# Optimization experiments

Measured on AMD Instinct MI355X. Metric: run time of the kernel, lower is better.

## Reference

```python
import jax, jax.numpy as jnp
import numpy as np

B, S, DIM, H = 8, 1024, 1024, 16
HID = 512  # FeedForward default hidden_dim=512 (module passes only dim)
DH = DIM // H
EPS = 1e-5


def setup_inputs() -> dict:
    key = jax.random.key(0)
    ks = jax.random.split(key, 12)
    s = 1.0 / np.sqrt(DIM)
    return {
        "x": jax.random.normal(ks[0], (B, S, DIM), dtype=jnp.float32),
        "Wq": jax.random.normal(ks[1], (DIM, DIM), dtype=jnp.float32) * s,
        "Wk": jax.random.normal(ks[2], (DIM, DIM), dtype=jnp.float32) * s,
        "Wv": jax.random.normal(ks[3], (DIM, DIM), dtype=jnp.float32) * s,
        "Wo": jax.random.normal(ks[4], (DIM, DIM), dtype=jnp.float32) * s,
        "ln1_g": jnp.ones((DIM,), jnp.float32),
        "ln1_b": jnp.zeros((DIM,), jnp.float32),
        "W1": jax.random.normal(ks[5], (DIM, HID), dtype=jnp.float32) * s,
        "b1": jnp.zeros((HID,), jnp.float32),
        "W2": jax.random.normal(ks[6], (HID, DIM), dtype=jnp.float32) * (1.0 / np.sqrt(HID)),
        "b2": jnp.zeros((DIM,), jnp.float32),
        "ln2_g": jnp.ones((DIM,), jnp.float32),
        "ln2_b": jnp.zeros((DIM,), jnp.float32),
    }


def _layer_norm(x, g, b):
    mu = jnp.mean(x, axis=-1, keepdims=True)
    var = jnp.mean(jnp.square(x - mu), axis=-1, keepdims=True)
    return (x - mu) * jax.lax.rsqrt(var + EPS) * g + b


def reference(x, Wq, Wk, Wv, Wo, ln1_g, ln1_b, W1, b1, W2, b2, ln2_g, ln2_b):
    # Multi-head self-attention (dropout = identity at eval)
    def heads(t):  # [B,S,DIM] -> [B,H,S,DH]
        return t.reshape(B, S, H, DH).transpose(0, 2, 1, 3)

    q = heads(x @ Wq)
    k = heads(x @ Wk)
    v = heads(x @ Wv)
    scores = jnp.einsum("bhqd,bhkd->bhqk", q, k) / jnp.sqrt(jnp.float32(DH))
    attn = jax.nn.softmax(scores, axis=-1)
    ctx = jnp.einsum("bhqk,bhkd->bhqd", attn, v)
    ctx = ctx.transpose(0, 2, 1, 3).reshape(B, S, DIM)
    mha = ctx @ Wo

    h = _layer_norm(mha + x, ln1_g, ln1_b)
    ff = jax.nn.relu(h @ W1 + b1) @ W2 + b2
    out = _layer_norm(ff + h, ln2_g, ln2_b)
    return out
```

## Files before the change

kernel.cpp:

```cpp
#include <hip/hip_runtime.h>
#include <cstdint>
#include <cstddef>

#define DEV __device__ __forceinline__

typedef __bf16 bf16x8 __attribute__((ext_vector_type(8)));
typedef __bf16 bf16x4 __attribute__((ext_vector_type(4)));
typedef short  short4v __attribute__((ext_vector_type(4)));
typedef float  f32x4  __attribute__((ext_vector_type(4)));

static constexpr int Bb  = 8;
static constexpr int S   = 1024;
static constexpr int DIM = 1024;
static constexpr int H   = 16;
static constexpr int DH  = 64;
static constexpr int HID = 512;
static constexpr int M   = Bb * S;

DEV uint16_t f2bf(float f) {
  union { float f; uint32_t u; } v; v.f = f;
  uint32_t r = v.u + 0x7fffu + ((v.u >> 16) & 1u);
  return (uint16_t)(r >> 16);
}
DEV float bf2f(uint32_t u) {
  union { uint32_t u; float f; } v; v.u = u << 16;
  return v.f;
}

DEV void gl_lds16(const uint16_t* g, uint16_t* lds) {
  __builtin_amdgcn_global_load_lds(
      (const __attribute__((address_space(1))) void*)g,
      (__attribute__((address_space(3))) void*)lds, 16, 0, 0);
}

DEV bf16x8 ld8(const uint16_t* p) { return *reinterpret_cast<const bf16x8*>(p); }

#if __has_builtin(__builtin_amdgcn_mfma_f32_16x16x16bf16_1k)
DEV f32x4 mfma16(bf16x4 a, bf16x4 b, f32x4 c) {
  return __builtin_amdgcn_mfma_f32_16x16x16bf16_1k(
      __builtin_bit_cast(short4v, a), __builtin_bit_cast(short4v, b), c, 0, 0, 0);
}
#else
DEV f32x4 mfma16(bf16x4 a, bf16x4 b, f32x4 c) {
  asm volatile("v_mfma_f32_16x16x16_bf16 %0, %1, %2, %0" : "+v"(c) : "v"(a), "v"(b));
  return c;
}
#endif

DEV int swz(int row, int col) {
  return row * 64 + (((col >> 3) ^ (row & 7)) << 3) + (col & 7);
}

__global__ __launch_bounds__(256) void cvt_f32_bf16(const float* __restrict__ in,
                                                    uint16_t* __restrict__ out, int n) {
  int i = (blockIdx.x * 256 + threadIdx.x) * 8;
  if (i >= n) return;
  const float4* p = reinterpret_cast<const float4*>(in + i);
  float4 a = p[0], b = p[1];
  uint16_t o[8] = {f2bf(a.x), f2bf(a.y), f2bf(a.z), f2bf(a.w),
                   f2bf(b.x), f2bf(b.y), f2bf(b.z), f2bf(b.w)};
  uint4 pk;
  pk.x = (uint32_t)o[0] | ((uint32_t)o[1] << 16);
  pk.y = (uint32_t)o[2] | ((uint32_t)o[3] << 16);
  pk.z = (uint32_t)o[4] | ((uint32_t)o[5] << 16);
  pk.w = (uint32_t)o[6] | ((uint32_t)o[7] << 16);
  *reinterpret_cast<uint4*>(out + i) = pk;
}

__global__ __launch_bounds__(256) void transpose_cvt(const float* __restrict__ in,
                                                     uint16_t* __restrict__ out,
                                                     int R, int C) {
  __shared__ float tile[32][33];
  int c0 = blockIdx.x * 32, r0 = blockIdx.y * 32;
  int tx = threadIdx.x, ty = threadIdx.y;
  #pragma unroll
  for (int i = 0; i < 4; i++)
    tile[ty + i * 8][tx] = in[(size_t)(r0 + ty + i * 8) * C + c0 + tx];
  __syncthreads();
  #pragma unroll
  for (int i = 0; i < 4; i++)
    out[(size_t)(c0 + ty + i * 8) * R + r0 + tx] = f2bf(tile[tx][ty + i * 8]);
}

__global__ __launch_bounds__(256) void vtrans(const uint16_t* __restrict__ qkv,
                                              uint16_t* __restrict__ vt) {
  int bh = blockIdx.x;
  int s0 = blockIdx.y * 64;
  int b = bh >> 4, h = bh & 15;
  int tid = threadIdx.x;
  __shared__ uint16_t t[64][65];
  #pragma unroll
  for (int j = 0; j < 16; j++) {
    int lin = j * 256 + tid;
    int sl = lin >> 6, d = lin & 63;
    t[d][sl] = qkv[(size_t)(b * S + s0 + sl) * 3072 + 2048 + h * 64 + d];
  }
  __syncthreads();
  #pragma unroll
  for (int j = 0; j < 16; j++) {
    int lin = j * 256 + tid;
    int dl = lin >> 6, sl = lin & 63;
    vt[((size_t)bh * 64 + dl) * S + s0 + sl] = t[dl][sl];
  }
}

template <int BIAS, int RELU, int OUT_BF16>
__global__ __launch_bounds__(256) void gemm_bt(const uint16_t* __restrict__ A,
                                               const uint16_t* __restrict__ Bt,
                                               const float* __restrict__ bias,
                                               void* __restrict__ Cout,
                                               int Mm, int N, int K) {
  __shared__ __align__(16) uint16_t As[128 * 32];
  __shared__ __align__(16) uint16_t Bs[128 * 32];
  const int tid = threadIdx.x;
  const int w = tid >> 6, l = tid & 63;
  int nwg = gridDim.x * gridDim.y;
  int lin = blockIdx.y * gridDim.x + blockIdx.x;
  if (!(nwg & 7)) lin = (lin & 7) * (nwg >> 3) + (lin >> 3);
  const int bx = lin % gridDim.x, by = lin / gridDim.x;
  const int m0 = by * 128, n0 = bx * 128;
  const int wr = (w >> 1) * 64, wc = (w & 1) * 64;
  const int wbase = w * 64;
  f32x4 acc[4][4] = {};
  const uint16_t* Ag = A + (size_t)m0 * K;
  const uint16_t* Bg = Bt + (size_t)n0 * K;

  for (int k0 = 0; k0 < K; k0 += 32) {
    __syncthreads();
    #pragma unroll
    for (int n = 0; n < 2; n++) {
      int lin2 = n * 256 + tid;
      int row = lin2 >> 2, col = (lin2 & 3) * 8;
      gl_lds16(Ag + (size_t)row * K + k0 + col, &As[(size_t)(n * 256 + wbase) * 8]);
      gl_lds16(Bg + (size_t)row * K + k0 + col, &Bs[(size_t)(n * 256 + wbase) * 8]);
    }
    __syncthreads();
    bf16x8 af[4], bfr[4];
    #pragma unroll
    for (int i = 0; i < 4; i++) {
      af[i]  = ld8(&As[(wr + i * 16 + (l & 15)) * 32 + (l >> 4) * 8]);
      bfr[i] = ld8(&Bs[(wc + i * 16 + (l & 15)) * 32 + (l >> 4) * 8]);
    }
    #pragma unroll
    for (int i = 0; i < 4; i++)
      #pragma unroll
      for (int j = 0; j < 4; j++)
        acc[i][j] = __builtin_amdgcn_mfma_f32_16x16x32_bf16(af[i], bfr[j], acc[i][j], 0, 0, 0);
  }

  const int r0 = m0 + wr + (l >> 4) * 4;
  const int c0 = n0 + wc + (l & 15);
  #pragma unroll
  for (int j = 0; j < 4; j++) {
    int col = c0 + j * 16;
    float bv = BIAS ? bias[col] : 0.0f;
    #pragma unroll
    for (int i = 0; i < 4; i++) {
      #pragma unroll
      for (int r = 0; r < 4; r++) {
        float v = acc[i][j][r] + bv;
        if (RELU) v = fmaxf(v, 0.0f);
        int row = r0 + i * 16 + r;
        if (OUT_BF16)
          ((uint16_t*)Cout)[(size_t)row * N + col] = f2bf(v);
        else
          ((float*)Cout)[(size_t)row * N + col] = v;
      }
    }
  }
}

__global__ __launch_bounds__(512, 2) void gemm256(const uint16_t* __restrict__ A,
                                                  const uint16_t* __restrict__ Bt,
                                                  uint16_t* __restrict__ Cout,
                                                  int N, int K) {
  __shared__ __align__(16) uint16_t As[2][256 * 64];
  __shared__ __align__(16) uint16_t Bs[2][256 * 64];
  const int tid = threadIdx.x;
  const int w = tid >> 6, l = tid & 63;
  const int hi = l >> 4, c = l & 15;
  int nwg = gridDim.x * gridDim.y;
  int lin = blockIdx.y * gridDim.x + blockIdx.x;
  if (!(nwg & 7)) lin = (lin & 7) * (nwg >> 3) + (lin >> 3);
  const int bx = lin % gridDim.x, by = lin / gridDim.x;
  const int m0 = by * 256, n0 = bx * 256;
  const int wr = w >> 2, wc = w & 3;
  const uint16_t* Ag = A + (size_t)m0 * K;
  const uint16_t* Bg = Bt + (size_t)n0 * K;
  f32x4 acc[8][4] = {};

  const int srow = tid >> 3, sch = tid & 7;
  auto stage = [&](int k0, int buf) {
    #pragma unroll
    for (int i = 0; i < 4; i++) {
      int row = i * 64 + srow;
      int scol = (sch ^ (row & 7)) * 8;
      gl_lds16(Ag + (size_t)row * K + k0 + scol, &As[buf][(i * 512 + w * 64) * 8]);
    }
    #pragma unroll
    for (int i = 0; i < 4; i++) {
      int row = i * 64 + srow;
      int scol = (sch ^ (row & 7)) * 8;
      gl_lds16(Bg + (size_t)row * K + k0 + scol, &Bs[buf][(i * 512 + w * 64) * 8]);
    }
  };

  stage(0, 0);
  stage(64, 1);
  asm volatile("s_waitcnt vmcnt(8)" ::: "memory");
  __builtin_amdgcn_s_barrier();

  const int NTK = K >> 6;
  for (int t = 0; t < NTK; t++) {
    const int cur = t & 1;
    const uint16_t* Ab = As[cur];
    const uint16_t* Bb = Bs[cur];
    bf16x8 bfr[4][2];
    #pragma unroll
    for (int ni = 0; ni < 4; ni++)
      #pragma unroll
      for (int kk = 0; kk < 2; kk++)
        bfr[ni][kk] = ld8(&Bb[swz(wc * 64 + ni * 16 + c, kk * 32 + hi * 8)]);
    #pragma unroll
    for (int mi = 0; mi < 8; mi++) {
      bf16x8 a0 = ld8(&Ab[swz(wr * 128 + mi * 16 + c, hi * 8)]);
      bf16x8 a1 = ld8(&Ab[swz(wr * 128 + mi * 16 + c, 32 + hi * 8)]);
      #pragma unroll
      for (int ni = 0; ni < 4; ni++) {
        acc[mi][ni] = __builtin_amdgcn_mfma_f32_16x16x32_bf16(a0, bfr[ni][0], acc[mi][ni], 0, 0, 0);
        acc[mi][ni] = __builtin_amdgcn_mfma_f32_16x16x32_bf16(a1, bfr[ni][1], acc[mi][ni], 0, 0, 0);
      }
    }
    if (t == NTK - 1) break;
    asm volatile("s_waitcnt lgkmcnt(0)" ::: "memory");
    __builtin_amdgcn_s_barrier();
    if (t + 2 < NTK) {
      stage((t + 2) << 6, cur);
      asm volatile("s_waitcnt vmcnt(8)" ::: "memory");
    } else {
      asm volatile("s_waitcnt vmcnt(0)" ::: "memory");
    }
    __builtin_amdgcn_s_barrier();
  }

  const int r0 = m0 + wr * 128 + hi * 4;
  const int c0 = n0 + wc * 64 + c;
  #pragma unroll
  for (int mi = 0; mi < 8; mi++)
    #pragma unroll
    for (int ni = 0; ni < 4; ni++)
      #pragma unroll
      for (int r = 0; r < 4; r++)
        Cout[(size_t)(r0 + mi * 16 + r) * N + c0 + ni * 16] = f2bf(acc[mi][ni][r]);
}

__global__ __launch_bounds__(256, 4) void attn5(const uint16_t* __restrict__ qkv,
                                                const uint16_t* __restrict__ vt,
                                                uint16_t* __restrict__ ctx) {
  int blk = blockIdx.x;
  int xcd = blk & 7, idx = blk >> 3;
  int qt = idx & 7;
  int bh = xcd + 8 * (idx >> 3);
  int h = bh & 15, b = bh >> 4;
  int q0 = qt * 128;
  int tid = threadIdx.x;
  int w = tid >> 6, l = tid & 63;
  int hi = l >> 4, c = l & 15;

  __shared__ __align__(16) uint16_t Klds[2][64 * 64];
  __shared__ __align__(16) uint16_t Vlds[2][64 * 64];

  const uint16_t* qbase = qkv + (size_t)(b * S + q0 + w * 32) * 3072 + h * 64;
  bf16x8 aq[2][2];
  #pragma unroll
  for (int qg = 0; qg < 2; qg++)
    #pragma unroll
    for (int dk = 0; dk < 2; dk++)
      aq[qg][dk] = ld8(qbase + (size_t)(qg * 16 + c) * 3072 + dk * 32 + hi * 8);

  f32x4 acc[2][4] = {};
  float psum[2] = {};

  const uint16_t* kgbase = qkv + (size_t)(b * S) * 3072 + 1024 + h * 64;
  const uint16_t* vgbase = vt + (size_t)(b * 16 + h) * 64 * S;

  int srow = tid >> 3, sch = tid & 7;
  uint4 kreg[2], vreg[2];

  auto load_tiles = [&](int kt) {
    #pragma unroll
    for (int i = 0; i < 2; i++) {
      int row = srow + i * 32;
      kreg[i] = *(const uint4*)(kgbase + (size_t)(kt + row) * 3072 + sch * 8);
      vreg[i] = *(const uint4*)(vgbase + (size_t)row * S + kt + sch * 8);
    }
  };
  auto store_tiles = [&](int buf) {
    #pragma unroll
    for (int i = 0; i < 2; i++) {
      int row = srow + i * 32;
      *(uint4*)&Klds[buf][swz(row, sch * 8)] = kreg[i];
      *(uint4*)&Vlds[buf][swz(row, sch * 8)] = vreg[i];
    }
  };

  load_tiles(0);
  store_tiles(0);
  __syncthreads();

  constexpr float C2 = 0.125f * 1.44269504f;
  constexpr int NT = S / 64;
  for (int t = 0; t < NT; t++) {
    int cur = t & 1;
    if (t + 1 < NT) load_tiles((t + 1) * 64);

    #pragma unroll
    for (int kb = 0; kb < 4; kb++) {
      bf16x8 kf0 = ld8(&Klds[cur][swz(kb * 16 + c, hi * 8)]);
      bf16x8 kf1 = ld8(&Klds[cur][swz(kb * 16 + c, 32 + hi * 8)]);
      bf16x4 pb[2];
      #pragma unroll
      for (int qg = 0; qg < 2; qg++) {
        f32x4 z = {0.f, 0.f, 0.f, 0.f};
        z = __builtin_amdgcn_mfma_f32_16x16x32_bf16(kf0, aq[qg][0], z, 0, 0, 0);
        z = __builtin_amdgcn_mfma_f32_16x16x32_bf16(kf1, aq[qg][1], z, 0, 0, 0);
        #pragma unroll
        for (int r = 0; r < 4; r++) {
          float p = exp2f(z[r] * C2);
          psum[qg] += p;
          pb[qg][r] = (__bf16)p;
        }
      }
      #pragma unroll
      for (int db = 0; db < 4; db++) {
        bf16x4 va = *(const bf16x4*)&Vlds[cur][swz(db * 16 + c, kb * 16 + hi * 4)];
        acc[0][db] = mfma16(va, pb[0], acc[0][db]);
        acc[1][db] = mfma16(va, pb[1], acc[1][db]);
      }
    }

    if (t + 1 < NT) store_tiles(cur ^ 1);
    __syncthreads();
  }

  #pragma unroll
  for (int qg = 0; qg < 2; qg++) {
    psum[qg] += __shfl_xor(psum[qg], 16);
    psum[qg] += __shfl_xor(psum[qg], 32);
  }

  uint16_t* Bw = &Vlds[w >> 1][(w & 1) * 2048];
  #pragma unroll
  for (int qg = 0; qg < 2; qg++) {
    float inv = 1.0f / psum[qg];
    int q = qg * 16 + c;
    #pragma unroll
    for (int db = 0; db < 4; db++) {
      uint2 pk;
      pk.x = (uint32_t)f2bf(acc[qg][db][0] * inv) |
             ((uint32_t)f2bf(acc[qg][db][1] * inv) << 16);
      pk.y = (uint32_t)f2bf(acc[qg][db][2] * inv) |
             ((uint32_t)f2bf(acc[qg][db][3] * inv) << 16);
      int chunk4 = (db * 4 + hi) ^ (q & 15);
      *(uint2*)&Bw[q * 64 + chunk4 * 4] = pk;
    }
  }
  int rrow = l >> 3, rch = l & 7;
  size_t gq0 = (size_t)(b * S + q0 + w * 32);
  #pragma unroll
  for (int it = 0; it < 4; it++) {
    int row = it * 8 + rrow;
    int k0 = (2 * rch) ^ (row & 15);
    int base = (k0 & ~1) * 4;
    uint4 v = *(const uint4*)&Bw[row * 64 + base];
    if (row & 1) { uint32_t t0 = v.x, t1 = v.y; v.x = v.z; v.y = v.w; v.z = t0; v.w = t1; }
    *(uint4*)&ctx[(gq0 + row) * DIM + h * 64 + rch * 8] = v;
  }
}

__global__ __launch_bounds__(256) void ln1_b(const uint16_t* __restrict__ a16,
                                             const float* __restrict__ xres,
                                             const float* __restrict__ g,
                                             const float* __restrict__ beta,
                                             uint16_t* __restrict__ h16) {
  int row = blockIdx.x;
  int t = threadIdx.x;
  int w = t >> 6, l = t & 63;
  uint2 av = reinterpret_cast<const uint2*>(a16 + (size_t)row * DIM)[t];
  float4 xv = reinterpret_cast<const float4*>(xres + (size_t)row * DIM)[t];
  float v0 = bf2f(av.x & 0xffff) + xv.x;
  float v1 = bf2f(av.x >> 16)    + xv.y;
  float v2 = bf2f(av.y & 0xffff) + xv.z;
  float v3 = bf2f(av.y >> 16)    + xv.w;
  float s = v0 + v1 + v2 + v3;
  float sq = v0 * v0 + v1 * v1 + v2 * v2 + v3 * v3;
  #pragma unroll
  for (int off = 32; off >= 1; off >>= 1) {
    s += __shfl_xor(s, off);
    sq += __shfl_xor(sq, off);
  }
  __shared__ float ws[4], wq[4];
  if (l == 0) { ws[w] = s; wq[w] = sq; }
  __syncthreads();
  s = ws[0] + ws[1] + ws[2] + ws[3];
  sq = wq[0] + wq[1] + wq[2] + wq[3];
  float mu = s * (1.0f / DIM);
  float var = sq * (1.0f / DIM) - mu * mu;
  float rstd = rsqrtf(var + 1e-5f);
  const float4 gv = reinterpret_cast<const float4*>(g)[t];
  const float4 btv = reinterpret_cast<const float4*>(beta)[t];
  float o0 = (v0 - mu) * rstd * gv.x + btv.x;
  float o1 = (v1 - mu) * rstd * gv.y + btv.y;
  float o2 = (v2 - mu) * rstd * gv.z + btv.z;
  float o3 = (v3 - mu) * rstd * gv.w + btv.w;
  uint2 pk;
  pk.x = (uint32_t)f2bf(o0) | ((uint32_t)f2bf(o1) << 16);
  pk.y = (uint32_t)f2bf(o2) | ((uint32_t)f2bf(o3) << 16);
  reinterpret_cast<uint2*>(h16 + (size_t)row * DIM)[t] = pk;
}

__global__ __launch_bounds__(256) void ln2_b(const float* __restrict__ ff,
                                             const uint16_t* __restrict__ h16,
                                             const float* __restrict__ g,
                                             const float* __restrict__ beta,
                                             float* __restrict__ out_f) {
  int row = blockIdx.x;
  int t = threadIdx.x;
  int w = t >> 6, l = t & 63;
  float4 av = reinterpret_cast<const float4*>(ff + (size_t)row * DIM)[t];
  uint2 hv = reinterpret_cast<const uint2*>(h16 + (size_t)row * DIM)[t];
  float v0 = av.x + bf2f(hv.x & 0xffff);
  float v1 = av.y + bf2f(hv.x >> 16);
  float v2 = av.z + bf2f(hv.y & 0xffff);
  float v3 = av.w + bf2f(hv.y >> 16);
  float s = v0 + v1 + v2 + v3;
  float sq = v0 * v0 + v1 * v1 + v2 * v2 + v3 * v3;
  #pragma unroll
  for (int off = 32; off >= 1; off >>= 1) {
    s += __shfl_xor(s, off);
    sq += __shfl_xor(sq, off);
  }
  __shared__ float ws[4], wq[4];
  if (l == 0) { ws[w] = s; wq[w] = sq; }
  __syncthreads();
  s = ws[0] + ws[1] + ws[2] + ws[3];
  sq = wq[0] + wq[1] + wq[2] + wq[3];
  float mu = s * (1.0f / DIM);
  float var = sq * (1.0f / DIM) - mu * mu;
  float rstd = rsqrtf(var + 1e-5f);
  const float4 gv = reinterpret_cast<const float4*>(g)[t];
  const float4 btv = reinterpret_cast<const float4*>(beta)[t];
  float4 o;
  o.x = (v0 - mu) * rstd * gv.x + btv.x;
  o.y = (v1 - mu) * rstd * gv.y + btv.y;
  o.z = (v2 - mu) * rstd * gv.z + btv.z;
  o.w = (v3 - mu) * rstd * gv.w + btv.w;
  reinterpret_cast<float4*>(out_f + (size_t)row * DIM)[t] = o;
}

extern "C" void kernel_launch(void* const* d_in, const int* in_sizes, int n_in,
                              void* d_out, int out_size, void* d_ws, size_t ws_size,
                              hipStream_t stream) {
  const float* x    = (const float*)d_in[0];
  const float* Wq   = (const float*)d_in[1];
  const float* Wk   = (const float*)d_in[2];
  const float* Wv   = (const float*)d_in[3];
  const float* Wo   = (const float*)d_in[4];
  const float* ln1g = (const float*)d_in[5];
  const float* ln1b = (const float*)d_in[6];
  const float* W1   = (const float*)d_in[7];
  const float* b1   = (const float*)d_in[8];
  const float* W2   = (const float*)d_in[9];
  const float* b2   = (const float*)d_in[10];
  const float* ln2g = (const float*)d_in[11];
  const float* ln2b = (const float*)d_in[12];
  float* out = (float*)d_out;

  char* ws = (char*)d_ws;
  uint16_t* wqkv_t = (uint16_t*)(ws + 0);
  uint16_t* wo_t   = (uint16_t*)(ws + 6291456);
  uint16_t* w1_t   = (uint16_t*)(ws + 8388608);
  uint16_t* w2_t   = (uint16_t*)(ws + 9437184);
  uint16_t* x16    = (uint16_t*)(ws + 10485760);
  uint16_t* ctx16  = x16;
  uint16_t* qkv16  = (uint16_t*)(ws + 27262976);
  uint16_t* mha16  = (uint16_t*)(ws + 27262976);
  float*    ff2    = (float*)(ws + 27262976);
  uint16_t* h16    = (uint16_t*)(ws + 60817408);
  uint16_t* vt16   = (uint16_t*)(ws + 77594624);
  uint16_t* mid16  = vt16;

  cvt_f32_bf16<<<4096, 256, 0, stream>>>(x, x16, M * DIM);
  dim3 tb(32, 8);
  transpose_cvt<<<dim3(32, 32), tb, 0, stream>>>(Wq, wqkv_t,                 DIM, DIM);
  transpose_cvt<<<dim3(32, 32), tb, 0, stream>>>(Wk, wqkv_t + 1024 * 1024,   DIM, DIM);
  transpose_cvt<<<dim3(32, 32), tb, 0, stream>>>(Wv, wqkv_t + 2048 * 1024,   DIM, DIM);
  transpose_cvt<<<dim3(32, 32), tb, 0, stream>>>(Wo, wo_t,                   DIM, DIM);
  transpose_cvt<<<dim3(16, 32), tb, 0, stream>>>(W1, w1_t, DIM, HID);
  transpose_cvt<<<dim3(32, 16), tb, 0, stream>>>(W2, w2_t, HID, DIM);
  gemm256<<<dim3(12, 32), 512, 0, stream>>>(x16, wqkv_t, qkv16, 3072, DIM);
  vtrans<<<dim3(128, 16), 256, 0, stream>>>(qkv16, vt16);
  attn5<<<1024, 256, 0, stream>>>(qkv16, vt16, ctx16);
  gemm_bt<0, 0, 1><<<dim3(8, 64), 256, 0, stream>>>(ctx16, wo_t, nullptr, mha16, M, DIM, DIM);
  ln1_b<<<M, 256, 0, stream>>>(mha16, x, ln1g, ln1b, h16);
  gemm_bt<1, 1, 1><<<dim3(4, 64), 256, 0, stream>>>(h16, w1_t, b1, mid16, M, HID, DIM);
  gemm_bt<1, 0, 0><<<dim3(8, 64), 256, 0, stream>>>(mid16, w2_t, b2, ff2, M, DIM, HID);
  ln2_b<<<M, 256, 0, stream>>>(ff2, h16, ln2g, ln2b, out);
}
```

Baseline: 275.4 us.

## Stage attention K/V tiles via direct global-to-LDS loads with deeper prefetch

The attention kernel now copies K and V tiles straight from global memory into LDS through a gl_lds16 helper, skipping the register round trip, and prefetches two tiles ahead with explicit vmcnt waits and barriers. It also interleaves the two QK MFMA chains, raises wave priority around the MFMA blocks, and bumps launch bounds to 5 blocks per CU. The goal is to hide global load latency and free registers for higher occupancy. The hand-written waitcnt and barrier sequence must stay correct, and the swizzle now depends on the load layout matching the swz() read pattern.

```diff
diff --git a/kernel.cpp b/kernel.cpp
--- a/kernel.cpp
+++ b/kernel.cpp
@@ -254,7 +254,7 @@
         Cout[(size_t)(r0 + mi * 16 + r) * N + c0 + ni * 16] = f2bf(acc[mi][ni][r]);
 }
 
-__global__ __launch_bounds__(256, 4) void attn5(const uint16_t* __restrict__ qkv,
+__global__ __launch_bounds__(256, 5) void attn6(const uint16_t* __restrict__ qkv,
                                                 const uint16_t* __restrict__ vt,
                                                 uint16_t* __restrict__ ctx) {
   int blk = blockIdx.x;
@@ -284,63 +284,71 @@
   const uint16_t* kgbase = qkv + (size_t)(b * S) * 3072 + 1024 + h * 64;
   const uint16_t* vgbase = vt + (size_t)(b * 16 + h) * 64 * S;
 
-  int srow = tid >> 3, sch = tid & 7;
-  uint4 kreg[2], vreg[2];
-
-  auto load_tiles = [&](int kt) {
+  const int lr = l >> 3, lc = l & 7;
+  const int scol = (lc ^ lr) * 8;
+  auto stage = [&](int kt, int buf) {
     #pragma unroll
     for (int i = 0; i < 2; i++) {
-      int row = srow + i * 32;
-      kreg[i] = *(const uint4*)(kgbase + (size_t)(kt + row) * 3072 + sch * 8);
-      vreg[i] = *(const uint4*)(vgbase + (size_t)row * S + kt + sch * 8);
+      int slab = w * 2 + i;
+      gl_lds16(kgbase + (size_t)(kt + slab * 8 + lr) * 3072 + scol,
+               &Klds[buf][slab * 512]);
+      gl_lds16(vgbase + (size_t)(slab * 8 + lr) * S + kt + scol,
+               &Vlds[buf][slab * 512]);
     }
   };
-  auto store_tiles = [&](int buf) {
-    #pragma unroll
-    for (int i = 0; i < 2; i++) {
-      int row = srow + i * 32;
-      *(uint4*)&Klds[buf][swz(row, sch * 8)] = kreg[i];
-      *(uint4*)&Vlds[buf][swz(row, sch * 8)] = vreg[i];
-    }
-  };
-
-  load_tiles(0);
-  store_tiles(0);
-  __syncthreads();
+
+  stage(0, 0);
+  stage(64, 1);
+  asm volatile("s_waitcnt vmcnt(4)" ::: "memory");
+  __builtin_amdgcn_s_barrier();
 
   constexpr float C2 = 0.125f * 1.44269504f;
   constexpr int NT = S / 64;
   for (int t = 0; t < NT; t++) {
     int cur = t & 1;
-    if (t + 1 < NT) load_tiles((t + 1) * 64);
-
+    const uint16_t* Kc = Klds[cur];
+    const uint16_t* Vc = Vlds[cur];
     #pragma unroll
     for (int kb = 0; kb < 4; kb++) {
-      bf16x8 kf0 = ld8(&Klds[cur][swz(kb * 16 + c, hi * 8)]);
-      bf16x8 kf1 = ld8(&Klds[cur][swz(kb * 16 + c, 32 + hi * 8)]);
+      bf16x8 kf0 = ld8(&Kc[swz(kb * 16 + c, hi * 8)]);
+      bf16x8 kf1 = ld8(&Kc[swz(kb * 16 + c, 32 + hi * 8)]);
       bf16x4 pb[2];
-      #pragma unroll
-      for (int qg = 0; qg < 2; qg++) {
-        f32x4 z = {0.f, 0.f, 0.f, 0.f};
-        z = __builtin_amdgcn_mfma_f32_16x16x32_bf16(kf0, aq[qg][0], z, 0, 0, 0);
-        z = __builtin_amdgcn_mfma_f32_16x16x32_bf16(kf1, aq[qg][1], z, 0, 0, 0);
-        #pragma unroll
-        for (int r = 0; r < 4; r++) {
-          float p = exp2f(z[r] * C2);
-          psum[qg] += p;
-          pb[qg][r] = (__bf16)p;
-        }
+      __builtin_amdgcn_s_setprio(1);
+      f32x4 z0 = {0.f, 0.f, 0.f, 0.f}, z1 = {0.f, 0.f, 0.f, 0.f};
+      z0 = __builtin_amdgcn_mfma_f32_16x16x32_bf16(kf0, aq[0][0], z0, 0, 0, 0);
+      z0 = __builtin_amdgcn_mfma_f32_16x16x32_bf16(kf1, aq[0][1], z0, 0, 0, 0);
+      z1 = __builtin_amdgcn_mfma_f32_16x16x32_bf16(kf0, aq[1][0], z1, 0, 0, 0);
+      z1 = __builtin_amdgcn_mfma_f32_16x16x32_bf16(kf1, aq[1][1], z1, 0, 0, 0);
+      __builtin_amdgcn_s_setprio(0);
+      #pragma unroll
+      for (int r = 0; r < 4; r++) {
+        float p0 = exp2f(z0[r] * C2);
+        float p1 = exp2f(z1[r] * C2);
+        psum[0] += p0;
+        psum[1] += p1;
+        pb[0][r] = (__bf16)p0;
+        pb[1][r] = (__bf16)p1;
       }
+      __builtin_amdgcn_s_setprio(1);
       #pragma unroll
       for (int db = 0; db < 4; db++) {
-        bf16x4 va = *(const bf16x4*)&Vlds[cur][swz(db * 16 + c, kb * 16 + hi * 4)];
+        bf16x4 va = *(const bf16x4*)&Vc[swz(db * 16 + c, kb * 16 + hi * 4)];
         acc[0][db] = mfma16(va, pb[0], acc[0][db]);
         acc[1][db] = mfma16(va, pb[1], acc[1][db]);
       }
-    }
-
-    if (t + 1 < NT) store_tiles(cur ^ 1);
-    __syncthreads();
+      __builtin_amdgcn_s_setprio(0);
+    }
+
+    if (t == NT - 1) break;
+    asm volatile("s_waitcnt lgkmcnt(0)" ::: "memory");
+    __builtin_amdgcn_s_barrier();
+    if (t + 2 < NT) {
+      stage((t + 2) * 64, cur);
+      asm volatile("s_waitcnt vmcnt(4)" ::: "memory");
+    } else {
+      asm volatile("s_waitcnt vmcnt(0)" ::: "memory");
+    }
+    __builtin_amdgcn_s_barrier();
   }
 
   #pragma unroll
@@ -348,6 +356,8 @@
     psum[qg] += __shfl_xor(psum[qg], 16);
     psum[qg] += __shfl_xor(psum[qg], 32);
   }
+
+  __syncthreads();
 
   uint16_t* Bw = &Vlds[w >> 1][(w & 1) * 2048];
   #pragma unroll
@@ -500,7 +510,7 @@
   transpose_cvt<<<dim3(32, 16), tb, 0, stream>>>(W2, w2_t, HID, DIM);
   gemm256<<<dim3(12, 32), 512, 0, stream>>>(x16, wqkv_t, qkv16, 3072, DIM);
   vtrans<<<dim3(128, 16), 256, 0, stream>>>(qkv16, vt16);
-  attn5<<<1024, 256, 0, stream>>>(qkv16, vt16, ctx16);
+  attn6<<<1024, 256, 0, stream>>>(qkv16, vt16, ctx16);
   gemm_bt<0, 0, 1><<<dim3(8, 64), 256, 0, stream>>>(ctx16, wo_t, nullptr, mha16, M, DIM, DIM);
   ln1_b<<<M, 256, 0, stream>>>(mha16, x, ln1g, ln1b, h16);
   gemm_bt<1, 1, 1><<<dim3(4, 64), 256, 0, stream>>>(h16, w1_t, b1, mid16, M, HID, DIM);
```

Measured after the change: 286.9 us. +4.2%, slower.

## Halve attention query tile per block and store FFN output in bf16

Applied to the files above, without the earlier changes.

The attention kernel now gives each wave 16 queries instead of 32, so a block covers 64 queries and the launch grows to 2048 blocks, with occupancy raised to 5 blocks per CU. This cuts register pressure and adds parallelism, but every block reloads the full K/V stream, so K/V traffic doubles. Separately, the second FFN GEMM now writes bf16 instead of fp32 and the final layernorm reads bf16, halving that intermediate's memory traffic at some precision cost.

```diff
diff --git a/kernel.cpp b/kernel.cpp
--- a/kernel.cpp
+++ b/kernel.cpp
@@ -254,15 +254,15 @@
         Cout[(size_t)(r0 + mi * 16 + r) * N + c0 + ni * 16] = f2bf(acc[mi][ni][r]);
 }
 
-__global__ __launch_bounds__(256, 4) void attn5(const uint16_t* __restrict__ qkv,
+__global__ __launch_bounds__(256, 5) void attn7(const uint16_t* __restrict__ qkv,
                                                 const uint16_t* __restrict__ vt,
                                                 uint16_t* __restrict__ ctx) {
   int blk = blockIdx.x;
   int xcd = blk & 7, idx = blk >> 3;
-  int qt = idx & 7;
-  int bh = xcd + 8 * (idx >> 3);
+  int qt = idx & 15;
+  int bh = xcd + 8 * (idx >> 4);
   int h = bh & 15, b = bh >> 4;
-  int q0 = qt * 128;
+  int q0 = qt * 64;
   int tid = threadIdx.x;
   int w = tid >> 6, l = tid & 63;
   int hi = l >> 4, c = l & 15;
@@ -270,16 +270,14 @@
   __shared__ __align__(16) uint16_t Klds[2][64 * 64];
   __shared__ __align__(16) uint16_t Vlds[2][64 * 64];
 
-  const uint16_t* qbase = qkv + (size_t)(b * S + q0 + w * 32) * 3072 + h * 64;
-  bf16x8 aq[2][2];
-  #pragma unroll
-  for (int qg = 0; qg < 2; qg++)
-    #pragma unroll
-    for (int dk = 0; dk < 2; dk++)
-      aq[qg][dk] = ld8(qbase + (size_t)(qg * 16 + c) * 3072 + dk * 32 + hi * 8);
-
-  f32x4 acc[2][4] = {};
-  float psum[2] = {};
+  const uint16_t* qbase = qkv + (size_t)(b * S + q0 + w * 16) * 3072 + h * 64;
+  bf16x8 aq[2];
+  #pragma unroll
+  for (int dk = 0; dk < 2; dk++)
+    aq[dk] = ld8(qbase + (size_t)c * 3072 + dk * 32 + hi * 8);
+
+  f32x4 acc[4] = {};
+  float psum = 0.0f;
 
   const uint16_t* kgbase = qkv + (size_t)(b * S) * 3072 + 1024 + h * 64;
   const uint16_t* vgbase = vt + (size_t)(b * 16 + h) * 64 * S;
@@ -313,29 +311,27 @@
   for (int t = 0; t < NT; t++) {
     int cur = t & 1;
     if (t + 1 < NT) load_tiles((t + 1) * 64);
+    const uint16_t* Kc = Klds[cur];
+    const uint16_t* Vc = Vlds[cur];
 
     #pragma unroll
     for (int kb = 0; kb < 4; kb++) {
-      bf16x8 kf0 = ld8(&Klds[cur][swz(kb * 16 + c, hi * 8)]);
-      bf16x8 kf1 = ld8(&Klds[cur][swz(kb * 16 + c, 32 + hi * 8)]);
-      bf16x4 pb[2];
-      #pragma unroll
-      for (int qg = 0; qg < 2; qg++) {
-        f32x4 z = {0.f, 0.f, 0.f, 0.f};
-        z = __builtin_amdgcn_mfma_f32_16x16x32_bf16(kf0, aq[qg][0], z, 0, 0, 0);
-        z = __builtin_amdgcn_mfma_f32_16x16x32_bf16(kf1, aq[qg][1], z, 0, 0, 0);
-        #pragma unroll
-        for (int r = 0; r < 4; r++) {
-          float p = exp2f(z[r] * C2);
-          psum[qg] += p;
-          pb[qg][r] = (__bf16)p;
-        }
+      bf16x8 kf0 = ld8(&Kc[swz(kb * 16 + c, hi * 8)]);
+      bf16x8 kf1 = ld8(&Kc[swz(kb * 16 + c, 32 + hi * 8)]);
+      f32x4 z = {0.f, 0.f, 0.f, 0.f};
+      z = __builtin_amdgcn_mfma_f32_16x16x32_bf16(kf0, aq[0], z, 0, 0, 0);
+      z = __builtin_amdgcn_mfma_f32_16x16x32_bf16(kf1, aq[1], z, 0, 0, 0);
+      bf16x4 pb;
+      #pragma unroll
+      for (int r = 0; r < 4; r++) {
+        float p = exp2f(z[r] * C2);
+        psum += p;
+        pb[r] = (__bf16)p;
       }
       #pragma unroll
       for (int db = 0; db < 4; db++) {
-        bf16x4 va = *(const bf16x4*)&Vlds[cur][swz(db * 16 + c, kb * 16 + hi * 4)];
-        acc[0][db] = mfma16(va, pb[0], acc[0][db]);
-        acc[1][db] = mfma16(va, pb[1], acc[1][db]);
+        bf16x4 va = *(const bf16x4*)&Vc[swz(db * 16 + c, kb * 16 + hi * 4)];
+        acc[db] = mfma16(va, pb, acc[db]);
       }
     }
 
@@ -343,34 +339,25 @@
     __syncthreads();
   }
 
-  #pragma unroll
-  for (int qg = 0; qg < 2; qg++) {
-    psum[qg] += __shfl_xor(psum[qg], 16);
-    psum[qg] += __shfl_xor(psum[qg], 32);
-  }
-
-  uint16_t* Bw = &Vlds[w >> 1][(w & 1) * 2048];
-  #pragma unroll
-  for (int qg = 0; qg < 2; qg++) {
-    float inv = 1.0f / psum[qg];
-    int q = qg * 16 + c;
-    #pragma unroll
-    for (int db = 0; db < 4; db++) {
-      uint2 pk;
-      pk.x = (uint32_t)f2bf(acc[qg][db][0] * inv) |
-             ((uint32_t)f2bf(acc[qg][db][1] * inv) << 16);
-      pk.y = (uint32_t)f2bf(acc[qg][db][2] * inv) |
-             ((uint32_t)f2bf(acc[qg][db][3] * inv) << 16);
-      int chunk4 = (db * 4 + hi) ^ (q & 15);
-      *(uint2*)&Bw[q * 64 + chunk4 * 4] = pk;
-    }
+  psum += __shfl_xor(psum, 16);
+  psum += __shfl_xor(psum, 32);
+  float inv = 1.0f / psum;
+
+  uint16_t* Bw = &Klds[0][w * 1024];
+  #pragma unroll
+  for (int db = 0; db < 4; db++) {
+    uint2 pk;
+    pk.x = (uint32_t)f2bf(acc[db][0] * inv) | ((uint32_t)f2bf(acc[db][1] * inv) << 16);
+    pk.y = (uint32_t)f2bf(acc[db][2] * inv) | ((uint32_t)f2bf(acc[db][3] * inv) << 16);
+    int chunk4 = (db * 4 + hi) ^ c;
+    *(uint2*)&Bw[c * 64 + chunk4 * 4] = pk;
   }
   int rrow = l >> 3, rch = l & 7;
-  size_t gq0 = (size_t)(b * S + q0 + w * 32);
-  #pragma unroll
-  for (int it = 0; it < 4; it++) {
+  size_t gq0 = (size_t)(b * S + q0 + w * 16);
+  #pragma unroll
+  for (int it = 0; it < 2; it++) {
     int row = it * 8 + rrow;
-    int k0 = (2 * rch) ^ (row & 15);
+    int k0 = (2 * rch) ^ row;
     int base = (k0 & ~1) * 4;
     uint4 v = *(const uint4*)&Bw[row * 64 + base];
     if (row & 1) { uint32_t t0 = v.x, t1 = v.y; v.x = v.z; v.y = v.w; v.z = t0; v.w = t1; }
@@ -419,7 +406,7 @@
   reinterpret_cast<uint2*>(h16 + (size_t)row * DIM)[t] = pk;
 }
 
-__global__ __launch_bounds__(256) void ln2_b(const float* __restrict__ ff,
+__global__ __launch_bounds__(256) void ln2_b(const uint16_t* __restrict__ ff16,
                                              const uint16_t* __restrict__ h16,
                                              const float* __restrict__ g,
                                              const float* __restrict__ beta,
@@ -427,12 +414,12 @@
   int row = blockIdx.x;
   int t = threadIdx.x;
   int w = t >> 6, l = t & 63;
-  float4 av = reinterpret_cast<const float4*>(ff + (size_t)row * DIM)[t];
+  uint2 av = reinterpret_cast<const uint2*>(ff16 + (size_t)row * DIM)[t];
   uint2 hv = reinterpret_cast<const uint2*>(h16 + (size_t)row * DIM)[t];
-  float v0 = av.x + bf2f(hv.x & 0xffff);
-  float v1 = av.y + bf2f(hv.x >> 16);
-  float v2 = av.z + bf2f(hv.y & 0xffff);
-  float v3 = av.w + bf2f(hv.y >> 16);
+  float v0 = bf2f(av.x & 0xffff) + bf2f(hv.x & 0xffff);
+  float v1 = bf2f(av.x >> 16)    + bf2f(hv.x >> 16);
+  float v2 = bf2f(av.y & 0xffff) + bf2f(hv.y & 0xffff);
+  float v3 = bf2f(av.y >> 16)    + bf2f(hv.y >> 16);
   float s = v0 + v1 + v2 + v3;
   float sq = v0 * v0 + v1 * v1 + v2 * v2 + v3 * v3;
   #pragma unroll
@@ -485,7 +472,7 @@
   uint16_t* ctx16  = x16;
   uint16_t* qkv16  = (uint16_t*)(ws + 27262976);
   uint16_t* mha16  = (uint16_t*)(ws + 27262976);
-  float*    ff2    = (float*)(ws + 27262976);
+  uint16_t* ff16   = (uint16_t*)(ws + 27262976);
   uint16_t* h16    = (uint16_t*)(ws + 60817408);
   uint16_t* vt16   = (uint16_t*)(ws + 77594624);
   uint16_t* mid16  = vt16;
@@ -500,10 +487,10 @@
   transpose_cvt<<<dim3(32, 16), tb, 0, stream>>>(W2, w2_t, HID, DIM);
   gemm256<<<dim3(12, 32), 512, 0, stream>>>(x16, wqkv_t, qkv16, 3072, DIM);
   vtrans<<<dim3(128, 16), 256, 0, stream>>>(qkv16, vt16);
-  attn5<<<1024, 256, 0, stream>>>(qkv16, vt16, ctx16);
+  attn7<<<2048, 256, 0, stream>>>(qkv16, vt16, ctx16);
   gemm_bt<0, 0, 1><<<dim3(8, 64), 256, 0, stream>>>(ctx16, wo_t, nullptr, mha16, M, DIM, DIM);
   ln1_b<<<M, 256, 0, stream>>>(mha16, x, ln1g, ln1b, h16);
   gemm_bt<1, 1, 1><<<dim3(4, 64), 256, 0, stream>>>(h16, w1_t, b1, mid16, M, HID, DIM);
-  gemm_bt<1, 0, 0><<<dim3(8, 64), 256, 0, stream>>>(mid16, w2_t, b2, ff2, M, DIM, HID);
-  ln2_b<<<M, 256, 0, stream>>>(ff2, h16, ln2g, ln2b, out);
-}
+  gemm_bt<1, 0, 1><<<dim3(8, 64), 256, 0, stream>>>(mid16, w2_t, b2, ff16, M, DIM, HID);
+  ln2_b<<<M, 256, 0, stream>>>(ff16, h16, ln2g, ln2b, out);
+}
```

Result: slower. 319.7 us (+16.1%).

## Merge prep kernels into one launch and use bf16 residual and FFN output

Applied to the files above, without the earlier changes.

Seven conversion and transpose launches are merged into one prep_all kernel that dispatches on block index. LN1 now reads the bf16 copy of x instead of fp32 x, and the second FFN GEMM writes bf16 output that LN2 reads. Because x16 must now survive until LN1, ctx gets its own workspace region. The aim is fewer launches and less memory traffic, at the cost of some precision in the residual and FFN output.

```diff
diff --git a/kernel.cpp b/kernel.cpp
--- a/kernel.cpp
+++ b/kernel.cpp
@@ -51,35 +51,60 @@
   return row * 64 + (((col >> 3) ^ (row & 7)) << 3) + (col & 7);
 }
 
-__global__ __launch_bounds__(256) void cvt_f32_bf16(const float* __restrict__ in,
-                                                    uint16_t* __restrict__ out, int n) {
-  int i = (blockIdx.x * 256 + threadIdx.x) * 8;
-  if (i >= n) return;
-  const float4* p = reinterpret_cast<const float4*>(in + i);
-  float4 a = p[0], b = p[1];
-  uint16_t o[8] = {f2bf(a.x), f2bf(a.y), f2bf(a.z), f2bf(a.w),
-                   f2bf(b.x), f2bf(b.y), f2bf(b.z), f2bf(b.w)};
-  uint4 pk;
-  pk.x = (uint32_t)o[0] | ((uint32_t)o[1] << 16);
-  pk.y = (uint32_t)o[2] | ((uint32_t)o[3] << 16);
-  pk.z = (uint32_t)o[4] | ((uint32_t)o[5] << 16);
-  pk.w = (uint32_t)o[6] | ((uint32_t)o[7] << 16);
-  *reinterpret_cast<uint4*>(out + i) = pk;
-}
-
-__global__ __launch_bounds__(256) void transpose_cvt(const float* __restrict__ in,
-                                                     uint16_t* __restrict__ out,
-                                                     int R, int C) {
+__global__ __launch_bounds__(256) void prep_all(const float* __restrict__ x,
+                                                uint16_t* __restrict__ x16,
+                                                const float* __restrict__ Wq,
+                                                const float* __restrict__ Wk,
+                                                const float* __restrict__ Wv,
+                                                const float* __restrict__ Wo,
+                                                const float* __restrict__ W1,
+                                                const float* __restrict__ W2,
+                                                uint16_t* __restrict__ wqkv_t,
+                                                uint16_t* __restrict__ wo_t,
+                                                uint16_t* __restrict__ w1_t,
+                                                uint16_t* __restrict__ w2_t) {
+  int bid = blockIdx.x;
+  int tid = threadIdx.x;
+  if (bid < 4096) {
+    int i = (bid * 256 + tid) * 8;
+    const float4* p = reinterpret_cast<const float4*>(x + i);
+    float4 a = p[0], b = p[1];
+    uint4 pk;
+    pk.x = (uint32_t)f2bf(a.x) | ((uint32_t)f2bf(a.y) << 16);
+    pk.y = (uint32_t)f2bf(a.z) | ((uint32_t)f2bf(a.w) << 16);
+    pk.z = (uint32_t)f2bf(b.x) | ((uint32_t)f2bf(b.y) << 16);
+    pk.w = (uint32_t)f2bf(b.z) | ((uint32_t)f2bf(b.w) << 16);
+    *reinterpret_cast<uint4*>(x16 + i) = pk;
+    return;
+  }
+  bid -= 4096;
+  const float* src;
+  uint16_t* dst;
+  int R, C, bx, by;
+  if (bid < 4096) {
+    int which = bid >> 10, id = bid & 1023;
+    if (which == 0)      { src = Wq; dst = wqkv_t; }
+    else if (which == 1) { src = Wk; dst = wqkv_t + 1048576; }
+    else if (which == 2) { src = Wv; dst = wqkv_t + 2097152; }
+    else                 { src = Wo; dst = wo_t; }
+    R = 1024; C = 1024; bx = id & 31; by = id >> 5;
+  } else if (bid < 4608) {
+    int id = bid - 4096;
+    src = W1; dst = w1_t; R = 1024; C = 512; bx = id & 15; by = id >> 4;
+  } else {
+    int id = bid - 4608;
+    src = W2; dst = w2_t; R = 512; C = 1024; bx = id & 31; by = id >> 5;
+  }
   __shared__ float tile[32][33];
-  int c0 = blockIdx.x * 32, r0 = blockIdx.y * 32;
-  int tx = threadIdx.x, ty = threadIdx.y;
+  int c0 = bx * 32, r0 = by * 32;
+  int tx = tid & 31, ty = tid >> 5;
   #pragma unroll
   for (int i = 0; i < 4; i++)
-    tile[ty + i * 8][tx] = in[(size_t)(r0 + ty + i * 8) * C + c0 + tx];
+    tile[ty + i * 8][tx] = src[(size_t)(r0 + ty + i * 8) * C + c0 + tx];
   __syncthreads();
   #pragma unroll
   for (int i = 0; i < 4; i++)
-    out[(size_t)(c0 + ty + i * 8) * R + r0 + tx] = f2bf(tile[tx][ty + i * 8]);
+    dst[(size_t)(c0 + ty + i * 8) * R + r0 + tx] = f2bf(tile[tx][ty + i * 8]);
 }
 
 __global__ __launch_bounds__(256) void vtrans(const uint16_t* __restrict__ qkv,
@@ -254,7 +279,7 @@
         Cout[(size_t)(r0 + mi * 16 + r) * N + c0 + ni * 16] = f2bf(acc[mi][ni][r]);
 }
 
-__global__ __launch_bounds__(256, 4) void attn5(const uint16_t* __restrict__ qkv,
+__global__ __launch_bounds__(256, 4) void attn8(const uint16_t* __restrict__ qkv,
                                                 const uint16_t* __restrict__ vt,
                                                 uint16_t* __restrict__ ctx) {
   int blk = blockIdx.x;
@@ -379,7 +404,7 @@
 }
 
 __global__ __launch_bounds__(256) void ln1_b(const uint16_t* __restrict__ a16,
-                                             const float* __restrict__ xres,
+                                             const uint16_t* __restrict__ x16,
                                              const float* __restrict__ g,
                                              const float* __restrict__ beta,
                                              uint16_t* __restrict__ h16) {
@@ -387,11 +412,11 @@
   int t = threadIdx.x;
   int w = t >> 6, l = t & 63;
   uint2 av = reinterpret_cast<const uint2*>(a16 + (size_t)row * DIM)[t];
-  float4 xv = reinterpret_cast<const float4*>(xres + (size_t)row * DIM)[t];
-  float v0 = bf2f(av.x & 0xffff) + xv.x;
-  float v1 = bf2f(av.x >> 16)    + xv.y;
-  float v2 = bf2f(av.y & 0xffff) + xv.z;
-  float v3 = bf2f(av.y >> 16)    + xv.w;
+  uint2 xv = reinterpret_cast<const uint2*>(x16 + (size_t)row * DIM)[t];
+  float v0 = bf2f(av.x & 0xffff) + bf2f(xv.x & 0xffff);
+  float v1 = bf2f(av.x >> 16)    + bf2f(xv.x >> 16);
+  float v2 = bf2f(av.y & 0xffff) + bf2f(xv.y & 0xffff);
+  float v3 = bf2f(av.y >> 16)    + bf2f(xv.y >> 16);
   float s = v0 + v1 + v2 + v3;
   float sq = v0 * v0 + v1 * v1 + v2 * v2 + v3 * v3;
   #pragma unroll
@@ -419,7 +444,7 @@
   reinterpret_cast<uint2*>(h16 + (size_t)row * DIM)[t] = pk;
 }
 
-__global__ __launch_bounds__(256) void ln2_b(const float* __restrict__ ff,
+__global__ __launch_bounds__(256) void ln2_b(const uint16_t* __restrict__ ff16,
                                              const uint16_t* __restrict__ h16,
                                              const float* __restrict__ g,
                                              const float* __restrict__ beta,
@@ -427,12 +452,12 @@
   int row = blockIdx.x;
   int t = threadIdx.x;
   int w = t >> 6, l = t & 63;
-  float4 av = reinterpret_cast<const float4*>(ff + (size_t)row * DIM)[t];
+  uint2 av = reinterpret_cast<const uint2*>(ff16 + (size_t)row * DIM)[t];
   uint2 hv = reinterpret_cast<const uint2*>(h16 + (size_t)row * DIM)[t];
-  float v0 = av.x + bf2f(hv.x & 0xffff);
-  float v1 = av.y + bf2f(hv.x >> 16);
-  float v2 = av.z + bf2f(hv.y & 0xffff);
-  float v3 = av.w + bf2f(hv.y >> 16);
+  float v0 = bf2f(av.x & 0xffff) + bf2f(hv.x & 0xffff);
+  float v1 = bf2f(av.x >> 16)    + bf2f(hv.x >> 16);
+  float v2 = bf2f(av.y & 0xffff) + bf2f(hv.y & 0xffff);
+  float v3 = bf2f(av.y >> 16)    + bf2f(hv.y >> 16);
   float s = v0 + v1 + v2 + v3;
   float sq = v0 * v0 + v1 * v1 + v2 * v2 + v3 * v3;
   #pragma unroll
@@ -482,28 +507,22 @@
   uint16_t* w1_t   = (uint16_t*)(ws + 8388608);
   uint16_t* w2_t   = (uint16_t*)(ws + 9437184);
   uint16_t* x16    = (uint16_t*)(ws + 10485760);
-  uint16_t* ctx16  = x16;
   uint16_t* qkv16  = (uint16_t*)(ws + 27262976);
   uint16_t* mha16  = (uint16_t*)(ws + 27262976);
-  float*    ff2    = (float*)(ws + 27262976);
+  uint16_t* ff16   = (uint16_t*)(ws + 27262976);
   uint16_t* h16    = (uint16_t*)(ws + 60817408);
   uint16_t* vt16   = (uint16_t*)(ws + 77594624);
   uint16_t* mid16  = vt16;
-
-  cvt_f32_bf16<<<4096, 256, 0, stream>>>(x, x16, M * DIM);
-  dim3 tb(32, 8);
-  transpose_cvt<<<dim3(32, 32), tb, 0, stream>>>(Wq, wqkv_t,                 DIM, DIM);
-  transpose_cvt<<<dim3(32, 32), tb, 0, stream>>>(Wk, wqkv_t + 1024 * 1024,   DIM, DIM);
-  transpose_cvt<<<dim3(32, 32), tb, 0, stream>>>(Wv, wqkv_t + 2048 * 1024,   DIM, DIM);
-  transpose_cvt<<<dim3(32, 32), tb, 0, stream>>>(Wo, wo_t,                   DIM, DIM);
-  transpose_cvt<<<dim3(16, 32), tb, 0, stream>>>(W1, w1_t, DIM, HID);
-  transpose_cvt<<<dim3(32, 16), tb, 0, stream>>>(W2, w2_t, HID, DIM);
+  uint16_t* ctx16  = (uint16_t*)(ws + 94371840);
+
+  prep_all<<<9216, 256, 0, stream>>>(x, x16, Wq, Wk, Wv, Wo, W1, W2,
+                                     wqkv_t, wo_t, w1_t, w2_t);
   gemm256<<<dim3(12, 32), 512, 0, stream>>>(x16, wqkv_t, qkv16, 3072, DIM);
   vtrans<<<dim3(128, 16), 256, 0, stream>>>(qkv16, vt16);
-  attn5<<<1024, 256, 0, stream>>>(qkv16, vt16, ctx16);
+  attn8<<<1024, 256, 0, stream>>>(qkv16, vt16, ctx16);
   gemm_bt<0, 0, 1><<<dim3(8, 64), 256, 0, stream>>>(ctx16, wo_t, nullptr, mha16, M, DIM, DIM);
-  ln1_b<<<M, 256, 0, stream>>>(mha16, x, ln1g, ln1b, h16);
+  ln1_b<<<M, 256, 0, stream>>>(mha16, x16, ln1g, ln1b, h16);
   gemm_bt<1, 1, 1><<<dim3(4, 64), 256, 0, stream>>>(h16, w1_t, b1, mid16, M, HID, DIM);
-  gemm_bt<1, 0, 0><<<dim3(8, 64), 256, 0, stream>>>(mid16, w2_t, b2, ff2, M, DIM, HID);
-  ln2_b<<<M, 256, 0, stream>>>(ff2, h16, ln2g, ln2b, out);
-}
+  gemm_bt<1, 0, 1><<<dim3(8, 64), 256, 0, stream>>>(mid16, w2_t, b2, ff16, M, DIM, HID);
+  ln2_b<<<M, 256, 0, stream>>>(ff16, h16, ln2g, ln2b, out);
+}
```

New measurement: 262.4 us. -4.7%, faster.
